# Performance work log

Hardware: AMD Instinct MI355X
Metric: run time of the kernel (lower is better)

## Reference

```python
import jax, jax.numpy as jnp
import numpy as np

DIM = 256
NUM_HEADS = 8
BALL_SIZE = 16
DIMENSIONALITY = 3
TOPK = 2  # hardcoded in the torch forward
NM = 8192  # n_balls(512) * ball_size(16)


def setup_inputs() -> dict:
    key = jax.random.key(0)
    ks = jax.random.split(key, 6)
    s = 0.02
    return {
        "x": jax.random.normal(ks[0], (NM, DIM), jnp.float32),
        "pos": jax.random.normal(ks[1], (NM, DIMENSIONALITY), jnp.float32),
        "W_qkv": jax.random.normal(ks[2], (3 * DIM, DIM), jnp.float32) * s,
        "b_qkv": jnp.zeros((3 * DIM,), jnp.float32),
        "W_pe": jax.random.normal(ks[3], (DIM, DIMENSIONALITY), jnp.float32) * s,
        "b_pe": jnp.zeros((DIM,), jnp.float32),
        "W_proj": jax.random.normal(ks[4], (DIM, DIM), jnp.float32) * s,
        "b_proj": jnp.zeros((DIM,), jnp.float32),
    }


def reference(x, pos, W_qkv, b_qkv, W_pe, b_pe, W_proj, b_proj):
    M, H, K = BALL_SIZE, NUM_HEADS, TOPK
    nm, dim = x.shape
    n = nm // M
    E = dim // H

    # relative positions wrt ball center (torch version is under no_grad)
    p = jax.lax.stop_gradient(pos).reshape(n, M, -1)
    rel = (p - p.mean(axis=1, keepdims=True)).reshape(nm, -1)
    x = x + rel @ W_pe.T + b_pe

    # qkv: '(n m) (H E K) -> K n H m E'  (K is innermost in the split)
    qkv = (x @ W_qkv.T + b_qkv).reshape(n, M, H, E, 3)
    qkv = jnp.transpose(qkv, (4, 0, 2, 1, 3))  # [3, n, H, m, E]
    q, k, v = qkv[0], qkv[1], qkv[2]

    qf = jnp.transpose(q, (1, 0, 2, 3)).reshape(H, nm, E)  # H (n m) E
    kh = jnp.transpose(k, (1, 0, 2, 3))  # H n m E
    vh = jnp.transpose(v, (1, 0, 2, 3))  # H n m E

    # per-ball key means, query-ball similarity, top-k ball selection
    kmean = kh.mean(axis=2)                          # H n E
    sim = jnp.einsum('hqe,hne->hqn', qf, kmean)      # H nm n
    _, idx = jax.lax.top_k(sim, K)                   # H nm K

    # gather selected balls' keys/values per (head, query-token)
    dk = jax.vmap(lambda kk, ii: kk[ii])(kh, idx).reshape(H, nm, K * M, E)
    dv = jax.vmap(lambda vv, ii: vv[ii])(vh, idx).reshape(H, nm, K * M, E)

    logits = jnp.einsum('hqe,hqke->hqk', qf, dk) / jnp.sqrt(jnp.float32(E))
    attn = jax.nn.softmax(logits, axis=-1)           # H nm (K*m)
    out = jnp.einsum('hqk,hqke->hqe', attn, dv)      # H nm E
    out = jnp.transpose(out, (1, 0, 2)).reshape(nm, dim)  # nm (H E)
    return out @ W_proj.T + b_proj
```

## Files before the change

kernel.cpp:

```cpp
#include <hip/hip_runtime.h>

#define DIM 256
#define NH 8
#define HE 32
#define BALL 16
#define NBALLS 512
#define NM 8192

typedef _Float16 f16x8 __attribute__((ext_vector_type(8)));
typedef float f32x4 __attribute__((ext_vector_type(4)));

__device__ __forceinline__ void f2h_split(float val, _Float16& hi,
                                          _Float16& lo) {
  hi = (_Float16)val;
  lo = (_Float16)(val - (float)hi);
}

__device__ __forceinline__ void gld_lds16(_Float16* lds, const _Float16* g) {
  __builtin_amdgcn_global_load_lds(
      (const __attribute__((address_space(1))) unsigned int*)g,
      (__attribute__((address_space(3))) unsigned int*)lds, 16, 0, 0);
}

__global__ __launch_bounds__(256) void k_prep(
    const float* __restrict__ x, const float* __restrict__ pos,
    const float* __restrict__ Wpe, const float* __restrict__ bpe,
    _Float16* __restrict__ xcat, const float* __restrict__ Wq,
    const float* __restrict__ Wp, _Float16* __restrict__ Bq,
    _Float16* __restrict__ Bp) {
  if (blockIdx.x >= NBALLS) {
    int n = blockIdx.x - NBALLS;
    int k = threadIdx.x;
    if (n < 768) {
      int c = n % 3, rr = n / 3;
      int e = rr & 31, h = rr >> 5;
      int np = c * 256 + h * 32 + e;
      _Float16 hi, lo;
      f2h_split(Wq[n * 256 + k], hi, lo);
      Bq[np * 768 + k] = hi;
      Bq[np * 768 + 256 + k] = hi;
      Bq[np * 768 + 512 + k] = lo;
    } else {
      int r = n - 768;
      _Float16 hi, lo;
      f2h_split(Wp[r * 256 + k], hi, lo);
      Bp[r * 768 + k] = hi;
      Bp[r * 768 + 256 + k] = hi;
      Bp[r * 768 + 512 + k] = lo;
    }
    return;
  }
  __shared__ float ps[BALL * 3];
  __shared__ float mean_s[3];
  int ball = blockIdx.x;
  int tid = threadIdx.x;
  if (tid < BALL * 3) ps[tid] = pos[ball * BALL * 3 + tid];
  __syncthreads();
  if (tid < 3) {
    float s = 0.f;
    for (int m = 0; m < BALL; ++m) s += ps[m * 3 + tid];
    mean_s[tid] = s * (1.f / BALL);
  }
  __syncthreads();
  int d = tid;
  float w0 = Wpe[d * 3 + 0], w1 = Wpe[d * 3 + 1], w2 = Wpe[d * 3 + 2];
  float bp = bpe[d];
  float m0 = mean_s[0], m1 = mean_s[1], m2 = mean_s[2];
  for (int m = 0; m < BALL; ++m) {
    int t = ball * BALL + m;
    float r0 = ps[m * 3 + 0] - m0;
    float r1 = ps[m * 3 + 1] - m1;
    float r2 = ps[m * 3 + 2] - m2;
    float val = x[t * DIM + d] + r0 * w0 + r1 * w1 + r2 * w2 + bp;
    _Float16 hi, lo;
    f2h_split(val, hi, lo);
    xcat[t * 512 + d] = hi;
    xcat[t * 512 + 256 + d] = lo;
  }
}

#define TBK 64

template <typename AF, typename BF, typename Epi>
__device__ __forceinline__ void gemm_core(AF a_addr, BF b_addr, int m0,
                                          int n0, Epi epi) {
  __shared__ _Float16 As[128 * 64];
  __shared__ _Float16 Bs[64 * 64];
  int tid = threadIdx.x;
  int w = tid >> 6, lane = tid & 63;
  int wm = (w >> 1) * 64, wn = (w & 1) * 32;
  int l15 = lane & 15, quad = lane >> 4;
  int sw = l15 & 7;
  f32x4 acc[4][2] = {};
  for (int k0 = 0; k0 < 768; k0 += TBK) {
    int ak0 = (k0 < 512) ? k0 : (k0 - 512);
    if (k0) __syncthreads();
#pragma unroll
    for (int t = 0; t < 4; ++t) {
      int f = tid + 256 * t;
      int row = f >> 3, sg = (f & 7) ^ (row & 7);
      gld_lds16(&As[f * 8], a_addr(m0 + row, ak0 + sg * 8));
    }
#pragma unroll
    for (int t = 0; t < 2; ++t) {
      int f = tid + 256 * t;
      int row = f >> 3, sg = (f & 7) ^ (row & 7);
      gld_lds16(&Bs[f * 8], b_addr(n0 + row, k0 + sg * 8));
    }
    __syncthreads();
#pragma unroll
    for (int kk = 0; kk < TBK; kk += 32) {
      int ls = (kk >> 3) + quad;
      int psg = (ls ^ sw) * 8;
      f16x8 bfr0 = *(const f16x8*)&Bs[(wn + l15) * 64 + psg];
      f16x8 bfr1 = *(const f16x8*)&Bs[(wn + 16 + l15) * 64 + psg];
#pragma unroll
      for (int mt = 0; mt < 4; ++mt) {
        f16x8 afr = *(const f16x8*)&As[(wm + mt * 16 + l15) * 64 + psg];
        acc[mt][0] = __builtin_amdgcn_mfma_f32_16x16x32_f16(afr, bfr0,
                                                            acc[mt][0], 0, 0,
                                                            0);
        acc[mt][1] = __builtin_amdgcn_mfma_f32_16x16x32_f16(afr, bfr1,
                                                            acc[mt][1], 0, 0,
                                                            0);
      }
    }
  }
  epi(acc, wm, wn, l15, quad);
}

__global__ __launch_bounds__(256) void k_qkv_gemm(
    const _Float16* __restrict__ A, const _Float16* __restrict__ B,
    const float* __restrict__ bias, _Float16* __restrict__ qcat,
    _Float16* __restrict__ kmc, _Float16* __restrict__ kv16) {
  int m0 = blockIdx.x * 128, n0 = blockIdx.y * 64;
  int c = n0 >> 8;
  gemm_core(
      [=](int r, int k) { return &A[r * 512 + k]; },
      [=](int r, int k) { return &B[r * 768 + k]; }, m0, n0,
      [=](f32x4 (&acc)[4][2], int wm, int wn, int l15, int quad) {
#pragma unroll
        for (int nt = 0; nt < 2; ++nt) {
          int col = n0 + wn + nt * 16 + l15;
          int cc = col & 255;
          int e = cc & 31, h = cc >> 5;
          float bv = bias[h * 96 + e * 3 + c];
#pragma unroll
          for (int mt = 0; mt < 4; ++mt) {
            int rb = m0 + wm + mt * 16;
            if (c == 0) {
#pragma unroll
              for (int r = 0; r < 4; ++r) {
                int row = rb + quad * 4 + r;
                _Float16 hi, lo;
                f2h_split(acc[mt][nt][r] + bv, hi, lo);
                qcat[(h * NM + row) * 64 + e] = hi;
                qcat[(h * NM + row) * 64 + 32 + e] = lo;
              }
            } else if (c == 1) {
              float s = 0.f;
#pragma unroll
              for (int r = 0; r < 4; ++r) {
                int row = rb + quad * 4 + r;
                float val = acc[mt][nt][r] + bv;
                kv16[(h * NM + row) * 64 + e] = (_Float16)val;
                s += acc[mt][nt][r];
              }
              s += __shfl_xor(s, 16);
              s += __shfl_xor(s, 32);
              if (quad == 0) {
                int ball = rb >> 4;
                _Float16 hi, lo;
                f2h_split(s * (1.f / BALL) + bv, hi, lo);
                kmc[(h * NBALLS + ball) * 64 + e] = hi;
                kmc[(h * NBALLS + ball) * 64 + 32 + e] = lo;
              }
            } else {
#pragma unroll
              for (int r = 0; r < 4; ++r) {
                int row = rb + quad * 4 + r;
                kv16[(h * NM + row) * 64 + 32 + e] =
                    (_Float16)(acc[mt][nt][r] + bv);
              }
            }
          }
        }
      });
}

__global__ __launch_bounds__(256) void k_proj(
    const _Float16* __restrict__ acat, const _Float16* __restrict__ B,
    const float* __restrict__ bias, float* __restrict__ out) {
  int m0 = blockIdx.x * 128, n0 = blockIdx.y * 64;
  gemm_core(
      [=](int r, int k) {
        int half = k >> 8, hh = (k >> 5) & 7, e0 = k & 31;
        return &acat[((half * NH + hh) * NM + r) * 32 + e0];
      },
      [=](int r, int k) { return &B[r * 768 + k]; }, m0, n0,
      [=](f32x4 (&acc)[4][2], int wm, int wn, int l15, int quad) {
#pragma unroll
        for (int nt = 0; nt < 2; ++nt) {
          int col = n0 + wn + nt * 16 + l15;
          float bv = bias[col];
#pragma unroll
          for (int mt = 0; mt < 4; ++mt) {
#pragma unroll
            for (int r = 0; r < 4; ++r) {
              int row = m0 + wm + mt * 16 + quad * 4 + r;
              out[row * DIM + col] = acc[mt][nt][r] + bv;
            }
          }
        }
      });
}

__global__ __launch_bounds__(512) void k_sim_topk(
    const _Float16* __restrict__ qcat, const _Float16* __restrict__ kmc,
    int2* __restrict__ topk2) {
  __shared__ _Float16 km_s[512 * 64];
  int tid = threadIdx.x;
  int bx = blockIdx.x;
  int h = bx & 7;
  int wv = tid >> 6, lane = tid & 63;
  int l15 = lane & 15, quad = lane >> 4;
  int sw = l15 & 7;
  int q0 = (bx >> 3) * 128 + wv * 16;

  const _Float16* qr = &qcat[(h * NM + q0 + l15) * 64];
  f16x8 qhi = *(const f16x8*)&qr[quad * 8];
  f16x8 qlo = *(const f16x8*)&qr[32 + quad * 8];

#pragma unroll
  for (int t = 0; t < 8; ++t) {
    int f = tid + 512 * t;
    int row = f >> 3, sg = (f & 7) ^ (row & 7);
    gld_lds16(&km_s[f * 8], &kmc[(h * NBALLS + row) * 64 + sg * 8]);
  }
  __syncthreads();

  float v0[4], v1[4];
  int i0[4], i1[4];
#pragma unroll
  for (int r = 0; r < 4; ++r) {
    v0[r] = -1e30f; v1[r] = -1e30f; i0[r] = 0; i1[r] = 0;
  }

#pragma unroll 4
  for (int tile = 0; tile < 32; ++tile) {
    const _Float16* bb = &km_s[(tile * 16 + l15) * 64];
    f16x8 bhi = *(const f16x8*)&bb[(quad ^ sw) * 8];
    f16x8 blo = *(const f16x8*)&bb[((4 + quad) ^ sw) * 8];
    f32x4 acc = {};
    acc = __builtin_amdgcn_mfma_f32_16x16x32_f16(qhi, bhi, acc, 0, 0, 0);
    acc = __builtin_amdgcn_mfma_f32_16x16x32_f16(qlo, bhi, acc, 0, 0, 0);
    acc = __builtin_amdgcn_mfma_f32_16x16x32_f16(qhi, blo, acc, 0, 0, 0);
    int ball = tile * 16 + l15;
#pragma unroll
    for (int r = 0; r < 4; ++r) {
      float s = acc[r];
      bool gt0 = s > v0[r];
      bool gt1 = s > v1[r];
      float nv1 = gt0 ? v0[r] : (gt1 ? s : v1[r]);
      int ni1 = gt0 ? i0[r] : (gt1 ? ball : i1[r]);
      v0[r] = gt0 ? s : v0[r];
      i0[r] = gt0 ? ball : i0[r];
      v1[r] = nv1;
      i1[r] = ni1;
    }
  }

#pragma unroll
  for (int m = 1; m < 16; m <<= 1) {
#pragma unroll
    for (int r = 0; r < 4; ++r) {
      float w0 = __shfl_xor(v0[r], m), w1 = __shfl_xor(v1[r], m);
      int j0 = __shfl_xor(i0[r], m), j1 = __shfl_xor(i1[r], m);
      bool a = w0 > v0[r];
      float c2v = a ? v0[r] : w0;
      int c2i = a ? i0[r] : j0;
      float o2v = a ? w1 : v1[r];
      int o2i = a ? j1 : i1[r];
      v0[r] = a ? w0 : v0[r];
      i0[r] = a ? j0 : i0[r];
      bool b2 = c2v > o2v;
      v1[r] = b2 ? c2v : o2v;
      i1[r] = b2 ? c2i : o2i;
    }
  }
  if (l15 == 0) {
#pragma unroll
    for (int r = 0; r < 4; ++r) {
      int q = q0 + quad * 4 + r;
      topk2[h * NM + q] = make_int2(i0[r], i1[r]);
    }
  }
}

__global__ __launch_bounds__(256) void k_attn(
    const _Float16* __restrict__ qcat, const _Float16* __restrict__ kv16,
    const int2* __restrict__ topk2, _Float16* __restrict__ acat) {
  __shared__ _Float16 kv_s[4][32 * 72];
  __shared__ float q_s[4][HE];
  __shared__ float attw[4][32];
  int wv = threadIdx.x >> 6;
  int tid = threadIdx.x & 63;
  int bx = blockIdx.x;
  int h = bx & 7;
  int t = (bx >> 3) * 4 + wv;

  int2 tk = topk2[h * NM + t];

  if (tid < HE) {
    const _Float16* qr = &qcat[(h * NM + t) * 64];
    q_s[wv][tid] = (float)qr[tid] + (float)qr[32 + tid];
  }
#pragma unroll
  for (int i = 0; i < 4; ++i) {
    int g = tid + 64 * i;
    int j = g >> 3, seg = g & 7;
    int ball = (j < 16) ? tk.x : tk.y;
    int m = j & 15;
    *(uint4*)&kv_s[wv][j * 72 + seg * 8] =
        *(const uint4*)&kv16[(h * NM + ball * BALL + m) * 64 + seg * 8];
  }

  int j = tid & 31, half = tid >> 5;
  int e0 = half * 16;
  float partial = 0.f;
  {
    f16x8 ka = *(const f16x8*)&kv_s[wv][j * 72 + e0];
    f16x8 kb = *(const f16x8*)&kv_s[wv][j * 72 + e0 + 8];
#pragma unroll
    for (int e = 0; e < 8; ++e) {
      partial += q_s[wv][e0 + e] * (float)ka[e];
      partial += q_s[wv][e0 + 8 + e] * (float)kb[e];
    }
  }
  partial += __shfl_xor(partial, 32);
  float logit = partial * 0.17677669529663687f;
  float mx = logit;
#pragma unroll
  for (int mk = 1; mk <= 16; mk <<= 1) mx = fmaxf(mx, __shfl_xor(mx, mk));
  float pexp = __expf(logit - mx);
  float sum = pexp;
#pragma unroll
  for (int mk = 1; mk <= 16; mk <<= 1) sum += __shfl_xor(sum, mk);
  float attn = pexp / sum;
  if (tid < 32) attw[wv][j] = attn;

  int e = tid & 31, j0 = half * 16;
  float po = 0.f;
#pragma unroll
  for (int jj = 0; jj < 16; ++jj)
    po += attw[wv][j0 + jj] * (float)kv_s[wv][(j0 + jj) * 72 + 32 + e];
  po += __shfl_xor(po, 32);
  if (tid < 32) {
    _Float16 hi, lo;
    f2h_split(po, hi, lo);
    acat[(h * NM + t) * 32 + e] = hi;
    acat[((NH + h) * NM + t) * 32 + e] = lo;
  }
}

extern "C" void kernel_launch(void* const* d_in, const int* in_sizes, int n_in,
                              void* d_out, int out_size, void* d_ws,
                              size_t ws_size, hipStream_t stream) {
  const float* x = (const float*)d_in[0];
  const float* pos = (const float*)d_in[1];
  const float* Wqkv = (const float*)d_in[2];
  const float* bqkv = (const float*)d_in[3];
  const float* Wpe = (const float*)d_in[4];
  const float* bpe = (const float*)d_in[5];
  const float* Wproj = (const float*)d_in[6];
  const float* bproj = (const float*)d_in[7];
  float* out = (float*)d_out;

  _Float16* kv16 = (_Float16*)d_ws;
  _Float16* qcat = kv16 + NH * NM * 64;
  _Float16* kmc = qcat + NH * NM * 64;
  int2* topk2 = (int2*)(kmc + NH * NBALLS * 64);
  _Float16* xcat = (_Float16*)(topk2 + NH * NM);
  _Float16* acat = xcat + NM * 512;
  _Float16* Bq = acat + 2 * NH * NM * 32;
  _Float16* Bp = Bq + 768 * 768;

  k_prep<<<NBALLS + 1024, 256, 0, stream>>>(x, pos, Wpe, bpe, xcat, Wqkv,
                                            Wproj, Bq, Bp);
  k_qkv_gemm<<<dim3(NM / 128, 768 / 64), 256, 0, stream>>>(xcat, Bq, bqkv,
                                                           qcat, kmc, kv16);
  k_sim_topk<<<NM / 128 * NH, 512, 0, stream>>>(qcat, kmc, topk2);
  k_attn<<<NH * NM / 4, 256, 0, stream>>>(qcat, kv16, topk2, acat);
  k_proj<<<dim3(NM / 128, DIM / 64), 256, 0, stream>>>(acat, Bp, bproj, out);
}
```

Baseline: 148.9 us.

## Fuse top-k selection with attention kernel and widen QKV GEMM tile to 96 columns

Merges the similarity/top-k kernel and the gather-attention kernel into one kernel. Top-k indices are passed between lanes by shuffles instead of being written to global memory, and queries are staged in LDS as fp32. This removes one launch and the topk2 round trip, but each wave now processes its 16 queries one after another, which lowers parallelism in the attention phase. The QKV GEMM is also templated on N-fragments and uses 96-column tiles, so fewer blocks each do more MFMA work per A tile load.

```diff
diff --git a/kernel.cpp b/kernel.cpp
--- a/kernel.cpp
+++ b/kernel.cpp
@@ -81,17 +81,17 @@
 
 #define TBK 64
 
-template <typename AF, typename BF, typename Epi>
+template <int NF, typename AF, typename BF, typename Epi>
 __device__ __forceinline__ void gemm_core(AF a_addr, BF b_addr, int m0,
                                           int n0, Epi epi) {
   __shared__ _Float16 As[128 * 64];
-  __shared__ _Float16 Bs[64 * 64];
+  __shared__ _Float16 Bs[32 * NF * 64];
   int tid = threadIdx.x;
   int w = tid >> 6, lane = tid & 63;
-  int wm = (w >> 1) * 64, wn = (w & 1) * 32;
+  int wm = (w >> 1) * 64, wn = (w & 1) * 16 * NF;
   int l15 = lane & 15, quad = lane >> 4;
   int sw = l15 & 7;
-  f32x4 acc[4][2] = {};
+  f32x4 acc[4][NF] = {};
   for (int k0 = 0; k0 < 768; k0 += TBK) {
     int ak0 = (k0 < 512) ? k0 : (k0 - 512);
     if (k0) __syncthreads();
@@ -102,7 +102,7 @@
       gld_lds16(&As[f * 8], a_addr(m0 + row, ak0 + sg * 8));
     }
 #pragma unroll
-    for (int t = 0; t < 2; ++t) {
+    for (int t = 0; t < NF; ++t) {
       int f = tid + 256 * t;
       int row = f >> 3, sg = (f & 7) ^ (row & 7);
       gld_lds16(&Bs[f * 8], b_addr(n0 + row, k0 + sg * 8));
@@ -112,17 +112,17 @@
     for (int kk = 0; kk < TBK; kk += 32) {
       int ls = (kk >> 3) + quad;
       int psg = (ls ^ sw) * 8;
-      f16x8 bfr0 = *(const f16x8*)&Bs[(wn + l15) * 64 + psg];
-      f16x8 bfr1 = *(const f16x8*)&Bs[(wn + 16 + l15) * 64 + psg];
+      f16x8 bfr[NF];
+#pragma unroll
+      for (int nt = 0; nt < NF; ++nt)
+        bfr[nt] = *(const f16x8*)&Bs[(wn + nt * 16 + l15) * 64 + psg];
 #pragma unroll
       for (int mt = 0; mt < 4; ++mt) {
         f16x8 afr = *(const f16x8*)&As[(wm + mt * 16 + l15) * 64 + psg];
-        acc[mt][0] = __builtin_amdgcn_mfma_f32_16x16x32_f16(afr, bfr0,
-                                                            acc[mt][0], 0, 0,
-                                                            0);
-        acc[mt][1] = __builtin_amdgcn_mfma_f32_16x16x32_f16(afr, bfr1,
-                                                            acc[mt][1], 0, 0,
-                                                            0);
+#pragma unroll
+        for (int nt = 0; nt < NF; ++nt)
+          acc[mt][nt] = __builtin_amdgcn_mfma_f32_16x16x32_f16(
+              afr, bfr[nt], acc[mt][nt], 0, 0, 0);
       }
     }
   }
@@ -133,18 +133,18 @@
     const _Float16* __restrict__ A, const _Float16* __restrict__ B,
     const float* __restrict__ bias, _Float16* __restrict__ qcat,
     _Float16* __restrict__ kmc, _Float16* __restrict__ kv16) {
-  int m0 = blockIdx.x * 128, n0 = blockIdx.y * 64;
-  int c = n0 >> 8;
-  gemm_core(
+  int m0 = blockIdx.x * 128, n0 = blockIdx.y * 96;
+  gemm_core<3>(
       [=](int r, int k) { return &A[r * 512 + k]; },
       [=](int r, int k) { return &B[r * 768 + k]; }, m0, n0,
-      [=](f32x4 (&acc)[4][2], int wm, int wn, int l15, int quad) {
-#pragma unroll
-        for (int nt = 0; nt < 2; ++nt) {
-          int col = n0 + wn + nt * 16 + l15;
-          int cc = col & 255;
-          int e = cc & 31, h = cc >> 5;
-          float bv = bias[h * 96 + e * 3 + c];
+      [=](f32x4 (&acc)[4][3], int wm, int wn, int l15, int quad) {
+#pragma unroll
+        for (int nt = 0; nt < 3; ++nt) {
+          int colbase = n0 + wn + nt * 16;
+          int c = colbase >> 8;
+          int cc = (colbase & 255) + l15;
+          int e = cc & 31, hh = cc >> 5;
+          float bv = bias[hh * 96 + e * 3 + c];
 #pragma unroll
           for (int mt = 0; mt < 4; ++mt) {
             int rb = m0 + wm + mt * 16;
@@ -154,8 +154,8 @@
                 int row = rb + quad * 4 + r;
                 _Float16 hi, lo;
                 f2h_split(acc[mt][nt][r] + bv, hi, lo);
-                qcat[(h * NM + row) * 64 + e] = hi;
-                qcat[(h * NM + row) * 64 + 32 + e] = lo;
+                qcat[(hh * NM + row) * 64 + e] = hi;
+                qcat[(hh * NM + row) * 64 + 32 + e] = lo;
               }
             } else if (c == 1) {
               float s = 0.f;
@@ -163,7 +163,7 @@
               for (int r = 0; r < 4; ++r) {
                 int row = rb + quad * 4 + r;
                 float val = acc[mt][nt][r] + bv;
-                kv16[(h * NM + row) * 64 + e] = (_Float16)val;
+                kv16[(hh * NM + row) * 64 + e] = (_Float16)val;
                 s += acc[mt][nt][r];
               }
               s += __shfl_xor(s, 16);
@@ -172,14 +172,14 @@
                 int ball = rb >> 4;
                 _Float16 hi, lo;
                 f2h_split(s * (1.f / BALL) + bv, hi, lo);
-                kmc[(h * NBALLS + ball) * 64 + e] = hi;
-                kmc[(h * NBALLS + ball) * 64 + 32 + e] = lo;
+                kmc[(hh * NBALLS + ball) * 64 + e] = hi;
+                kmc[(hh * NBALLS + ball) * 64 + 32 + e] = lo;
               }
             } else {
 #pragma unroll
               for (int r = 0; r < 4; ++r) {
                 int row = rb + quad * 4 + r;
-                kv16[(h * NM + row) * 64 + 32 + e] =
+                kv16[(hh * NM + row) * 64 + 32 + e] =
                     (_Float16)(acc[mt][nt][r] + bv);
               }
             }
@@ -192,7 +192,7 @@
     const _Float16* __restrict__ acat, const _Float16* __restrict__ B,
     const float* __restrict__ bias, float* __restrict__ out) {
   int m0 = blockIdx.x * 128, n0 = blockIdx.y * 64;
-  gemm_core(
+  gemm_core<2>(
       [=](int r, int k) {
         int half = k >> 8, hh = (k >> 5) & 7, e0 = k & 31;
         return &acat[((half * NH + hh) * NM + r) * 32 + e0];
@@ -215,17 +215,29 @@
       });
 }
 
-__global__ __launch_bounds__(512) void k_sim_topk(
+__global__ __launch_bounds__(512) void k_simattn(
     const _Float16* __restrict__ qcat, const _Float16* __restrict__ kmc,
-    int2* __restrict__ topk2) {
-  __shared__ _Float16 km_s[512 * 64];
+    const _Float16* __restrict__ kv16, _Float16* __restrict__ acat) {
+  __shared__ _Float16 smem[40960];
+  _Float16* km_s = smem;
+  float* q_all = (float*)(smem + 32768);
+
   int tid = threadIdx.x;
   int bx = blockIdx.x;
   int h = bx & 7;
+  int q0b = (bx >> 3) * 128;
   int wv = tid >> 6, lane = tid & 63;
   int l15 = lane & 15, quad = lane >> 4;
   int sw = l15 & 7;
-  int q0 = (bx >> 3) * 128 + wv * 16;
+  int q0 = q0b + wv * 16;
+
+#pragma unroll
+  for (int t = 0; t < 8; ++t) {
+    int p = tid + 512 * t;
+    int q = p >> 5, e = p & 31;
+    const _Float16* qp = &qcat[(h * NM + q0b + q) * 64];
+    q_all[q * 32 + e] = (float)qp[e] + (float)qp[32 + e];
+  }
 
   const _Float16* qr = &qcat[(h * NM + q0 + l15) * 64];
   f16x8 qhi = *(const f16x8*)&qr[quad * 8];
@@ -288,78 +300,66 @@
       i1[r] = b2 ? c2i : o2i;
     }
   }
-  if (l15 == 0) {
-#pragma unroll
-    for (int r = 0; r < 4; ++r) {
-      int q = q0 + quad * 4 + r;
-      topk2[h * NM + q] = make_int2(i0[r], i1[r]);
-    }
-  }
-}
-
-__global__ __launch_bounds__(256) void k_attn(
-    const _Float16* __restrict__ qcat, const _Float16* __restrict__ kv16,
-    const int2* __restrict__ topk2, _Float16* __restrict__ acat) {
-  __shared__ _Float16 kv_s[4][32 * 72];
-  __shared__ float q_s[4][HE];
-  __shared__ float attw[4][32];
-  int wv = threadIdx.x >> 6;
-  int tid = threadIdx.x & 63;
-  int bx = blockIdx.x;
-  int h = bx & 7;
-  int t = (bx >> 3) * 4 + wv;
-
-  int2 tk = topk2[h * NM + t];
-
-  if (tid < HE) {
-    const _Float16* qr = &qcat[(h * NM + t) * 64];
-    q_s[wv][tid] = (float)qr[tid] + (float)qr[32 + tid];
-  }
-#pragma unroll
-  for (int i = 0; i < 4; ++i) {
-    int g = tid + 64 * i;
-    int j = g >> 3, seg = g & 7;
-    int ball = (j < 16) ? tk.x : tk.y;
-    int m = j & 15;
-    *(uint4*)&kv_s[wv][j * 72 + seg * 8] =
-        *(const uint4*)&kv16[(h * NM + ball * BALL + m) * 64 + seg * 8];
-  }
-
-  int j = tid & 31, half = tid >> 5;
-  int e0 = half * 16;
-  float partial = 0.f;
-  {
-    f16x8 ka = *(const f16x8*)&kv_s[wv][j * 72 + e0];
-    f16x8 kb = *(const f16x8*)&kv_s[wv][j * 72 + e0 + 8];
-#pragma unroll
-    for (int e = 0; e < 8; ++e) {
-      partial += q_s[wv][e0 + e] * (float)ka[e];
-      partial += q_s[wv][e0 + 8 + e] * (float)kb[e];
-    }
-  }
-  partial += __shfl_xor(partial, 32);
-  float logit = partial * 0.17677669529663687f;
-  float mx = logit;
-#pragma unroll
-  for (int mk = 1; mk <= 16; mk <<= 1) mx = fmaxf(mx, __shfl_xor(mx, mk));
-  float pexp = __expf(logit - mx);
-  float sum = pexp;
-#pragma unroll
-  for (int mk = 1; mk <= 16; mk <<= 1) sum += __shfl_xor(sum, mk);
-  float attn = pexp / sum;
-  if (tid < 32) attw[wv][j] = attn;
-
-  int e = tid & 31, j0 = half * 16;
-  float po = 0.f;
-#pragma unroll
-  for (int jj = 0; jj < 16; ++jj)
-    po += attw[wv][j0 + jj] * (float)kv_s[wv][(j0 + jj) * 72 + 32 + e];
-  po += __shfl_xor(po, 32);
-  if (tid < 32) {
-    _Float16 hi, lo;
-    f2h_split(po, hi, lo);
-    acat[(h * NM + t) * 32 + e] = hi;
-    acat[((NH + h) * NM + t) * 32 + e] = lo;
+
+  __syncthreads();
+
+  _Float16* kv_s = &smem[wv * 2304];
+  float* attw = (float*)(smem + 18432) + wv * 32;
+
+#pragma unroll
+  for (int qi = 0; qi < 16; ++qi) {
+    int src = (qi >> 2) << 4;
+    int b0 = __shfl(i0[qi & 3], src);
+    int b1 = __shfl(i1[qi & 3], src);
+    int t = q0 + qi;
+
+#pragma unroll
+    for (int i = 0; i < 4; ++i) {
+      int g = lane + 64 * i;
+      int j = g >> 3, seg = g & 7;
+      int ball = (j < 16) ? b0 : b1;
+      int m = j & 15;
+      *(uint4*)&kv_s[j * 72 + seg * 8] =
+          *(const uint4*)&kv16[(h * NM + ball * BALL + m) * 64 + seg * 8];
+    }
+
+    int j = lane & 31, half = lane >> 5;
+    int e0 = half * 16;
+    const float* qv = &q_all[(wv * 16 + qi) * 32];
+    float partial = 0.f;
+    {
+      f16x8 ka = *(const f16x8*)&kv_s[j * 72 + e0];
+      f16x8 kb = *(const f16x8*)&kv_s[j * 72 + e0 + 8];
+#pragma unroll
+      for (int e = 0; e < 8; ++e) {
+        partial += qv[e0 + e] * (float)ka[e];
+        partial += qv[e0 + 8 + e] * (float)kb[e];
+      }
+    }
+    partial += __shfl_xor(partial, 32);
+    float logit = partial * 0.17677669529663687f;
+    float mx = logit;
+#pragma unroll
+    for (int mk = 1; mk <= 16; mk <<= 1) mx = fmaxf(mx, __shfl_xor(mx, mk));
+    float pexp = __expf(logit - mx);
+    float sum = pexp;
+#pragma unroll
+    for (int mk = 1; mk <= 16; mk <<= 1) sum += __shfl_xor(sum, mk);
+    float attn = pexp / sum;
+    if (lane < 32) attw[j] = attn;
+
+    int e = lane & 31, j0 = half * 16;
+    float po = 0.f;
+#pragma unroll
+    for (int jj = 0; jj < 16; ++jj)
+      po += attw[j0 + jj] * (float)kv_s[(j0 + jj) * 72 + 32 + e];
+    po += __shfl_xor(po, 32);
+    if (lane < 32) {
+      _Float16 hi, lo;
+      f2h_split(po, hi, lo);
+      acat[(h * NM + t) * 32 + e] = hi;
+      acat[((NH + h) * NM + t) * 32 + e] = lo;
+    }
   }
 }
 
@@ -379,17 +379,15 @@
   _Float16* kv16 = (_Float16*)d_ws;
   _Float16* qcat = kv16 + NH * NM * 64;
   _Float16* kmc = qcat + NH * NM * 64;
-  int2* topk2 = (int2*)(kmc + NH * NBALLS * 64);
-  _Float16* xcat = (_Float16*)(topk2 + NH * NM);
+  _Float16* xcat = kmc + NH * NBALLS * 64;
   _Float16* acat = xcat + NM * 512;
   _Float16* Bq = acat + 2 * NH * NM * 32;
   _Float16* Bp = Bq + 768 * 768;
 
   k_prep<<<NBALLS + 1024, 256, 0, stream>>>(x, pos, Wpe, bpe, xcat, Wqkv,
                                             Wproj, Bq, Bp);
-  k_qkv_gemm<<<dim3(NM / 128, 768 / 64), 256, 0, stream>>>(xcat, Bq, bqkv,
+  k_qkv_gemm<<<dim3(NM / 128, 768 / 96), 256, 0, stream>>>(xcat, Bq, bqkv,
                                                            qcat, kmc, kv16);
-  k_sim_topk<<<NM / 128 * NH, 512, 0, stream>>>(qcat, kmc, topk2);
-  k_attn<<<NH * NM / 4, 256, 0, stream>>>(qcat, kv16, topk2, acat);
+  k_simattn<<<NM / 128 * NH, 512, 0, stream>>>(qcat, kmc, kv16, acat);
   k_proj<<<dim3(NM / 128, DIM / 64), 256, 0, stream>>>(acat, Bp, bproj, out);
 }
```

After: 152.8 us. +2.6%, slower.
